# Kernel optimization log

Measured on AMD Instinct MI355X. Metric: run time of the kernel, lower is better.

Reference implementation:

```python
import jax, jax.numpy as jnp
import numpy as np

NUM_CLASSES = 24


def setup_inputs() -> dict:
    key = jax.random.key(0)
    k1, k2 = jax.random.split(key)
    data = jax.random.normal(k1, (8, 128, 128, 128), dtype=jnp.float32)
    label = jax.random.randint(k2, (8, 512, 512), 0, NUM_CLASSES, dtype=jnp.int64)
    return {"data": data, "label": label}


def reference(data, label):
    B, C, h, w = data.shape
    _, H, W = label.shape
    # nearest-neighbor interpolate to (H, W): torch 'nearest' uses floor(dst * src/dst)
    ri = (jnp.arange(H) * h) // H
    ci = (jnp.arange(W) * w) // W
    data_up = data[:, :, ri[:, None], ci[None, :]]  # [B, C, H, W]
    valid = label != -1                              # ignore mask
    lab = jnp.where(valid, label, 0)
    # scatter-add instead of one-hot + einsum (same math)
    seg = (lab + jnp.arange(B, dtype=lab.dtype)[:, None, None] * NUM_CLASSES).reshape(-1)
    x = (data_up * valid[:, None, :, :].astype(data.dtype))  # zero out ignored pixels
    x = x.transpose(0, 2, 3, 1).reshape(B * H * W, C)        # [B*H*W, C]
    sums = jax.ops.segment_sum(x, seg, num_segments=B * NUM_CLASSES)
    sums = sums.reshape(B, NUM_CLASSES, C)                   # [B, N, C]
    counts = jax.ops.segment_sum(valid.reshape(-1).astype(jnp.float32), seg,
                                 num_segments=B * NUM_CLASSES)
    counts = counts.reshape(B, NUM_CLASSES)                  # [B, N]
    feature = (sums / (counts[:, :, None] + 1e-8)).transpose(0, 2, 1)  # [B, C, N]
    mask = (counts > 0).astype(jnp.float32)                  # [B, N]
    return feature, mask
```

## Files before the change

### kernel.cpp

```cpp
#include <hip/hip_runtime.h>

#define NCLS 24
#define NB 8
#define NCH 128
#define WLO 128
#define WHI 512
#define CELLS (128*128)
#define SUBS 2
#define BPB 128
#define NBLK (NB * BPB)
#define KCH (NCLS * NCH)
#define NF (NB * KCH)

typedef _Float16 f16x4 __attribute__((ext_vector_type(4)));
typedef _Float16 f16x8 __attribute__((ext_vector_type(8)));
typedef float    f32x4 __attribute__((ext_vector_type(4)));

#define HSWZ(c_, e_) ((e_) ^ (((c_) & 7) << 3))

__global__ __launch_bounds__(256, 4)
void fm_main(const float* __restrict__ data, const int* __restrict__ label,
             _Float16* __restrict__ part, float* __restrict__ cpart)
{
    __shared__ float    histf[32 * 64];
    __shared__ _Float16 tile[NCH * 64];

    const int bid  = blockIdx.x;
    const int b    = bid >> 7;
    const int grp  = bid & 127;
    const int tid  = threadIdx.x;

    const int q    = tid & 15;
    const int chb  = tid >> 4;
    const int r    = tid >> 6;
    const int cl   = tid & 63;
    const int w    = tid >> 6;
    const int lane = tid & 63;

    const float* dbase = data  + (size_t)b * NCH * CELLS;
    const int*   lbase = label + (size_t)b * (WHI * WHI) + (size_t)(4 * grp + r) * WHI;

    float4 v[8];
    int4 lv;
    {
        const int cb = grp * WLO;
#pragma unroll
        for (int k = 0; k < 8; ++k)
            v[k] = *reinterpret_cast<const float4*>(dbase + (size_t)(chb + k * 16) * CELLS + cb + q * 4);
        lv = *reinterpret_cast<const int4*>(lbase + cl * 4);
    }

    f32x4 acc[2][2];
#pragma unroll
    for (int mt = 0; mt < 2; ++mt)
#pragma unroll
        for (int nt = 0; nt < 2; ++nt) acc[mt][nt] = (f32x4){0.f, 0.f, 0.f, 0.f};
    float cs0 = 0.f, cs1 = 0.f;

#pragma unroll
    for (int s = 0; s < SUBS; ++s) {
#pragma unroll
        for (int k = 0; k < 8; ++k) histf[tid + k * 256] = 0.f;
        __syncthreads();

        if ((unsigned)lv.x < 24u) atomicAdd(&histf[lv.x * 64 + HSWZ(lv.x, cl)], 1.f);
        if ((unsigned)lv.y < 24u) atomicAdd(&histf[lv.y * 64 + HSWZ(lv.y, cl)], 1.f);
        if ((unsigned)lv.z < 24u) atomicAdd(&histf[lv.z * 64 + HSWZ(lv.z, cl)], 1.f);
        if ((unsigned)lv.w < 24u) atomicAdd(&histf[lv.w * 64 + HSWZ(lv.w, cl)], 1.f);

#pragma unroll
        for (int k = 0; k < 8; ++k) {
            const int ch = chb + k * 16;
            f16x4 hv;
            hv[0] = (_Float16)v[k].x; hv[1] = (_Float16)v[k].y;
            hv[2] = (_Float16)v[k].z; hv[3] = (_Float16)v[k].w;
            const int idx = ch * 64 + ((((q >> 1) ^ (ch & 7)) << 3) | ((q & 1) << 2));
            *reinterpret_cast<f16x4*>(&tile[idx]) = hv;
        }

        if (s + 1 < SUBS) {
            const int cb = grp * WLO + 64;
#pragma unroll
            for (int k = 0; k < 8; ++k)
                v[k] = *reinterpret_cast<const float4*>(dbase + (size_t)(chb + k * 16) * CELLS + cb + q * 4);
            lv = *reinterpret_cast<const int4*>(lbase + 256 + cl * 4);
        }
        __syncthreads();

        f16x8 af[2][2];
#pragma unroll
        for (int mt = 0; mt < 2; ++mt)
#pragma unroll
            for (int kt = 0; kt < 2; ++kt) {
                const int cls = mt * 16 + (lane & 15);
                const int e0  = kt * 32 + (lane >> 4) * 8;
                const float* hp = &histf[cls * 64 + HSWZ(cls, e0)];
                const f32x4 h0 = *reinterpret_cast<const f32x4*>(hp);
                const f32x4 h1 = *reinterpret_cast<const f32x4*>(hp + 4);
                f16x8 a;
                a[0] = (_Float16)h0.x; a[1] = (_Float16)h0.y; a[2] = (_Float16)h0.z; a[3] = (_Float16)h0.w;
                a[4] = (_Float16)h1.x; a[5] = (_Float16)h1.y; a[6] = (_Float16)h1.z; a[7] = (_Float16)h1.w;
                af[mt][kt] = a;
                const float p = (h0.x + h0.y) + (h0.z + h0.w) + (h1.x + h1.y) + (h1.z + h1.w);
                if (mt == 0) cs0 += p; else cs1 += p;
            }

        f16x8 bf[2][2];
#pragma unroll
        for (int nt = 0; nt < 2; ++nt)
#pragma unroll
            for (int kt = 0; kt < 2; ++kt) {
                const int row = w * 32 + nt * 16 + (lane & 15);
                const int g   = kt * 4 + (lane >> 4);
                bf[nt][kt] = *reinterpret_cast<const f16x8*>(&tile[row * 64 + ((g ^ (row & 7)) << 3)]);
            }

#pragma unroll
        for (int mt = 0; mt < 2; ++mt)
#pragma unroll
            for (int nt = 0; nt < 2; ++nt)
#pragma unroll
                for (int kt = 0; kt < 2; ++kt)
                    acc[mt][nt] = __builtin_amdgcn_mfma_f32_16x16x32_f16(
                        af[mt][kt], bf[nt][kt], acc[mt][nt], 0, 0, 0);

        if (s + 1 < SUBS) __syncthreads();
    }

    cs0 += __shfl_xor(cs0, 16, 64); cs0 += __shfl_xor(cs0, 32, 64);
    cs1 += __shfl_xor(cs1, 16, 64); cs1 += __shfl_xor(cs1, 32, 64);
    if (w == 0 && lane < 16) {
        cpart[(size_t)bid * NCLS + lane] = cs0;
        if (lane < 8) cpart[(size_t)bid * NCLS + 16 + lane] = cs1;
    }

    _Float16* pblk = part + (size_t)bid * KCH;
#pragma unroll
    for (int mt = 0; mt < 2; ++mt)
#pragma unroll
        for (int nt = 0; nt < 2; ++nt)
#pragma unroll
            for (int rg = 0; rg < 4; ++rg) {
                const int cls = mt * 16 + (lane >> 4) * 4 + rg;
                const int ch  = w * 32 + nt * 16 + (lane & 15);
                if (cls < NCLS) pblk[cls * NCH + ch] = (_Float16)acc[mt][nt][rg];
            }
}

__global__ __launch_bounds__(256)
void fm_final(const _Float16* __restrict__ part, const float* __restrict__ cpart,
              float* __restrict__ out)
{
    __shared__ float red[256];
    __shared__ float credv[128];
    const int bid  = blockIdx.x;
    const int b    = bid / (NCLS * 2);
    const int rem  = bid % (NCLS * 2);
    const int cls  = rem >> 1;
    const int half = rem & 1;
    const int t    = threadIdx.x;
    const int c    = t & 63;
    const int gq   = t >> 6;

    if (t < 128) credv[t] = cpart[(size_t)(b * BPB + t) * NCLS + cls];

    const _Float16* pb = part + (size_t)(b * BPB + gq * 32) * KCH + cls * NCH + half * 64 + c;
    float s = 0.f;
#pragma unroll 8
    for (int g = 0; g < 32; ++g) s += (float)pb[(size_t)g * KCH];
    red[t] = s;
    __syncthreads();

    if (t < 64) {
        float cnt = credv[t] + credv[t + 64];
#pragma unroll
        for (int o = 32; o >= 1; o >>= 1) cnt += __shfl_xor(cnt, o, 64);
        const float sf = red[t] + red[t + 64] + red[t + 128] + red[t + 192];
        out[(size_t)b * KCH + (half * 64 + t) * NCLS + cls] = sf / (cnt + 1e-8f);
        if (t == 0 && half == 0) out[NF + b * NCLS + cls] = (cnt > 0.f) ? 1.f : 0.f;
    }
}

extern "C" void kernel_launch(void* const* d_in, const int* in_sizes, int n_in,
                              void* d_out, int out_size, void* d_ws, size_t ws_size,
                              hipStream_t stream) {
    const float* data  = (const float*)d_in[0];
    const int*   label = (const int*)d_in[1];
    float*     out   = (float*)d_out;
    _Float16*  part  = (_Float16*)d_ws;
    float*     cpart = (float*)(part + (size_t)NBLK * KCH);

    fm_main<<<dim3(NBLK), dim3(256), 0, stream>>>(data, label, part, cpart);
    fm_final<<<dim3(NB * NCLS * 2), dim3(256), 0, stream>>>(part, cpart, out);
}
```

Before: 27.37 us.

## Split label histogram into separate kernel and stream weights through global memory

```diff
diff --git a/kernel.cpp b/kernel.cpp
--- a/kernel.cpp
+++ b/kernel.cpp
@@ -3,148 +3,147 @@
 #define NCLS 24
 #define NB 8
 #define NCH 128
-#define WLO 128
 #define WHI 512
 #define CELLS (128*128)
-#define SUBS 2
-#define BPB 128
-#define NBLK (NB * BPB)
-#define KCH (NCLS * NCH)
+#define CPB 256
+#define KBLK 64
+#define NBLK (NB * KBLK)
+#define MROW 32
+#define KCH (NCH * NCLS)
 #define NF (NB * KCH)
+#define RP 129
+#define WSTR ((size_t)MROW * CELLS)
 
-typedef _Float16 f16x4 __attribute__((ext_vector_type(4)));
 typedef _Float16 f16x8 __attribute__((ext_vector_type(8)));
 typedef float    f32x4 __attribute__((ext_vector_type(4)));
 
-#define HSWZ(c_, e_) ((e_) ^ (((c_) & 7) << 3))
+__global__ __launch_bounds__(256)
+void fm_wcount(const int* __restrict__ label, _Float16* __restrict__ W,
+               float* __restrict__ cpart)
+{
+    __shared__ float h[NCLS * 257];
+    __shared__ float ps[NCLS * 8];
+    const int bid = blockIdx.x, b = bid >> 6, cblk = bid & 63;
+    const int t = threadIdx.x;
+    const int cell = cblk * 256 + t;
+    const int y = cell >> 7, x = cell & 127;
 
-__global__ __launch_bounds__(256, 4)
-void fm_main(const float* __restrict__ data, const int* __restrict__ label,
-             _Float16* __restrict__ part, float* __restrict__ cpart)
+#pragma unroll
+    for (int k = 0; k < 25; ++k) {
+        const int idx = t + k * 256;
+        if (idx < NCLS * 257) h[idx] = 0.f;
+    }
+    __syncthreads();
+
+    const int* lp = label + (size_t)b * (WHI * WHI) + (size_t)(4 * y) * WHI + 4 * x;
+    const int4 L0 = *(const int4*)lp;
+    const int4 L1 = *(const int4*)(lp + WHI);
+    const int4 L2 = *(const int4*)(lp + 2 * WHI);
+    const int4 L3 = *(const int4*)(lp + 3 * WHI);
+#define AH(v) if ((unsigned)(v) < 24u) atomicAdd(&h[(v) * 257 + t], 1.f)
+    AH(L0.x); AH(L0.y); AH(L0.z); AH(L0.w);
+    AH(L1.x); AH(L1.y); AH(L1.z); AH(L1.w);
+    AH(L2.x); AH(L2.y); AH(L2.z); AH(L2.w);
+    AH(L3.x); AH(L3.y); AH(L3.z); AH(L3.w);
+#undef AH
+
+#pragma unroll
+    for (int cls = 0; cls < NCLS; ++cls)
+        W[(size_t)b * WSTR + (size_t)cls * CELLS + cell] = (_Float16)h[cls * 257 + t];
+
+    __syncthreads();
+    if (t < 192) {
+        const int cls = t >> 3, seg = t & 7;
+        float s = 0.f;
+#pragma unroll
+        for (int m = 0; m < 32; ++m) s += h[cls * 257 + seg + 8 * m];
+        ps[cls * 8 + seg] = s;
+    }
+    __syncthreads();
+    if (t < NCLS) {
+        float s = 0.f;
+#pragma unroll
+        for (int g = 0; g < 8; ++g) s += ps[t * 8 + g];
+        cpart[bid * NCLS + t] = s;
+    }
+}
+
+__global__ __launch_bounds__(256, 2)
+void fm_gemm(const float* __restrict__ data, const _Float16* __restrict__ W,
+             _Float16* __restrict__ part)
 {
-    __shared__ float    histf[32 * 64];
-    __shared__ _Float16 tile[NCH * 64];
+    __shared__ float red[4 * MROW * RP];
+    const int bid = blockIdx.x, b = bid >> 6, kblk = bid & 63;
+    const int tid = threadIdx.x, w = tid >> 6, l = tid & 63;
+    const int l15 = l & 15, lg = l >> 4;
+    const int c0 = kblk * CPB + w * 64;
 
-    const int bid  = blockIdx.x;
-    const int b    = bid >> 7;
-    const int grp  = bid & 127;
-    const int tid  = threadIdx.x;
-
-    const int q    = tid & 15;
-    const int chb  = tid >> 4;
-    const int r    = tid >> 6;
-    const int cl   = tid & 63;
-    const int w    = tid >> 6;
-    const int lane = tid & 63;
-
-    const float* dbase = data  + (size_t)b * NCH * CELLS;
-    const int*   lbase = label + (size_t)b * (WHI * WHI) + (size_t)(4 * grp + r) * WHI;
-
-    float4 v[8];
-    int4 lv;
-    {
-        const int cb = grp * WLO;
-#pragma unroll
-        for (int k = 0; k < 8; ++k)
-            v[k] = *reinterpret_cast<const float4*>(dbase + (size_t)(chb + k * 16) * CELLS + cb + q * 4);
-        lv = *reinterpret_cast<const int4*>(lbase + cl * 4);
-    }
-
-    f32x4 acc[2][2];
+    f16x8 af[2][2];
 #pragma unroll
     for (int mt = 0; mt < 2; ++mt)
 #pragma unroll
-        for (int nt = 0; nt < 2; ++nt) acc[mt][nt] = (f32x4){0.f, 0.f, 0.f, 0.f};
-    float cs0 = 0.f, cs1 = 0.f;
+        for (int kt = 0; kt < 2; ++kt)
+            af[mt][kt] = *(const f16x8*)(W + (size_t)b * WSTR
+                                           + (size_t)(mt * 16 + l15) * CELLS
+                                           + c0 + kt * 32 + lg * 8);
 
+    f32x4 bs[2][8][2];
 #pragma unroll
-    for (int s = 0; s < SUBS; ++s) {
+    for (int kt = 0; kt < 2; ++kt)
 #pragma unroll
-        for (int k = 0; k < 8; ++k) histf[tid + k * 256] = 0.f;
-        __syncthreads();
+        for (int n = 0; n < 8; ++n)
+#pragma unroll
+            for (int p = 0; p < 2; ++p)
+                bs[kt][n][p] = *(const f32x4*)(data + (size_t)(b * NCH + n * 16 + l15) * CELLS
+                                                 + c0 + kt * 32 + lg * 8 + p * 4);
+    __builtin_amdgcn_sched_barrier(0);
 
-        if ((unsigned)lv.x < 24u) atomicAdd(&histf[lv.x * 64 + HSWZ(lv.x, cl)], 1.f);
-        if ((unsigned)lv.y < 24u) atomicAdd(&histf[lv.y * 64 + HSWZ(lv.y, cl)], 1.f);
-        if ((unsigned)lv.z < 24u) atomicAdd(&histf[lv.z * 64 + HSWZ(lv.z, cl)], 1.f);
-        if ((unsigned)lv.w < 24u) atomicAdd(&histf[lv.w * 64 + HSWZ(lv.w, cl)], 1.f);
-
-#pragma unroll
-        for (int k = 0; k < 8; ++k) {
-            const int ch = chb + k * 16;
-            f16x4 hv;
-            hv[0] = (_Float16)v[k].x; hv[1] = (_Float16)v[k].y;
-            hv[2] = (_Float16)v[k].z; hv[3] = (_Float16)v[k].w;
-            const int idx = ch * 64 + ((((q >> 1) ^ (ch & 7)) << 3) | ((q & 1) << 2));
-            *reinterpret_cast<f16x4*>(&tile[idx]) = hv;
-        }
-
-        if (s + 1 < SUBS) {
-            const int cb = grp * WLO + 64;
-#pragma unroll
-            for (int k = 0; k < 8; ++k)
-                v[k] = *reinterpret_cast<const float4*>(dbase + (size_t)(chb + k * 16) * CELLS + cb + q * 4);
-            lv = *reinterpret_cast<const int4*>(lbase + 256 + cl * 4);
-        }
-        __syncthreads();
-
-        f16x8 af[2][2];
-#pragma unroll
-        for (int mt = 0; mt < 2; ++mt)
-#pragma unroll
-            for (int kt = 0; kt < 2; ++kt) {
-                const int cls = mt * 16 + (lane & 15);
-                const int e0  = kt * 32 + (lane >> 4) * 8;
-                const float* hp = &histf[cls * 64 + HSWZ(cls, e0)];
-                const f32x4 h0 = *reinterpret_cast<const f32x4*>(hp);
-                const f32x4 h1 = *reinterpret_cast<const f32x4*>(hp + 4);
-                f16x8 a;
-                a[0] = (_Float16)h0.x; a[1] = (_Float16)h0.y; a[2] = (_Float16)h0.z; a[3] = (_Float16)h0.w;
-                a[4] = (_Float16)h1.x; a[5] = (_Float16)h1.y; a[6] = (_Float16)h1.z; a[7] = (_Float16)h1.w;
-                af[mt][kt] = a;
-                const float p = (h0.x + h0.y) + (h0.z + h0.w) + (h1.x + h1.y) + (h1.z + h1.w);
-                if (mt == 0) cs0 += p; else cs1 += p;
-            }
-
-        f16x8 bf[2][2];
-#pragma unroll
-        for (int nt = 0; nt < 2; ++nt)
-#pragma unroll
-            for (int kt = 0; kt < 2; ++kt) {
-                const int row = w * 32 + nt * 16 + (lane & 15);
-                const int g   = kt * 4 + (lane >> 4);
-                bf[nt][kt] = *reinterpret_cast<const f16x8*>(&tile[row * 64 + ((g ^ (row & 7)) << 3)]);
-            }
-
-#pragma unroll
-        for (int mt = 0; mt < 2; ++mt)
-#pragma unroll
-            for (int nt = 0; nt < 2; ++nt)
-#pragma unroll
-                for (int kt = 0; kt < 2; ++kt)
-                    acc[mt][nt] = __builtin_amdgcn_mfma_f32_16x16x32_f16(
-                        af[mt][kt], bf[nt][kt], acc[mt][nt], 0, 0, 0);
-
-        if (s + 1 < SUBS) __syncthreads();
-    }
-
-    cs0 += __shfl_xor(cs0, 16, 64); cs0 += __shfl_xor(cs0, 32, 64);
-    cs1 += __shfl_xor(cs1, 16, 64); cs1 += __shfl_xor(cs1, 32, 64);
-    if (w == 0 && lane < 16) {
-        cpart[(size_t)bid * NCLS + lane] = cs0;
-        if (lane < 8) cpart[(size_t)bid * NCLS + 16 + lane] = cs1;
-    }
-
-    _Float16* pblk = part + (size_t)bid * KCH;
+    f32x4 acc[2][8];
 #pragma unroll
     for (int mt = 0; mt < 2; ++mt)
 #pragma unroll
-        for (int nt = 0; nt < 2; ++nt)
+        for (int n = 0; n < 8; ++n) acc[mt][n] = (f32x4){0.f, 0.f, 0.f, 0.f};
+
 #pragma unroll
-            for (int rg = 0; rg < 4; ++rg) {
-                const int cls = mt * 16 + (lane >> 4) * 4 + rg;
-                const int ch  = w * 32 + nt * 16 + (lane & 15);
-                if (cls < NCLS) pblk[cls * NCH + ch] = (_Float16)acc[mt][nt][rg];
+    for (int kt = 0; kt < 2; ++kt)
+#pragma unroll
+        for (int n = 0; n < 8; ++n) {
+            f16x8 bf;
+            bf[0] = (_Float16)bs[kt][n][0].x; bf[1] = (_Float16)bs[kt][n][0].y;
+            bf[2] = (_Float16)bs[kt][n][0].z; bf[3] = (_Float16)bs[kt][n][0].w;
+            bf[4] = (_Float16)bs[kt][n][1].x; bf[5] = (_Float16)bs[kt][n][1].y;
+            bf[6] = (_Float16)bs[kt][n][1].z; bf[7] = (_Float16)bs[kt][n][1].w;
+            acc[0][n] = __builtin_amdgcn_mfma_f32_16x16x32_f16(af[0][kt], bf, acc[0][n], 0, 0, 0);
+            acc[1][n] = __builtin_amdgcn_mfma_f32_16x16x32_f16(af[1][kt], bf, acc[1][n], 0, 0, 0);
+        }
+
+    float* rw = &red[w * MROW * RP];
+#pragma unroll
+    for (int mt = 0; mt < 2; ++mt)
+#pragma unroll
+        for (int n = 0; n < 8; ++n)
+#pragma unroll
+            for (int rg = 0; rg < 4; ++rg)
+                rw[(mt * 16 + lg * 4 + rg) * RP + n * 16 + l15] = acc[mt][n][rg];
+    __syncthreads();
+
+    const int p = tid & 63, clsg = tid >> 6;
+#pragma unroll
+    for (int i = 0; i < 8; ++i) {
+        const int cls = clsg * 8 + i;
+        if (cls < NCLS) {
+            float s0 = 0.f, s1 = 0.f;
+#pragma unroll
+            for (int wv = 0; wv < 4; ++wv) {
+                s0 += red[wv * MROW * RP + cls * RP + 2 * p];
+                s1 += red[wv * MROW * RP + cls * RP + 2 * p + 1];
             }
+            const _Float16 h0 = (_Float16)s0, h1 = (_Float16)s1;
+            unsigned u = (unsigned)*(const unsigned short*)&h0
+                       | ((unsigned)*(const unsigned short*)&h1 << 16);
+            *(unsigned*)(part + (size_t)bid * 4096 + cls * 128 + 2 * p) = u;
+        }
+    }
 }
 
 __global__ __launch_bounds__(256)
@@ -152,27 +151,23 @@
               float* __restrict__ out)
 {
     __shared__ float red[256];
-    __shared__ float credv[128];
-    const int bid  = blockIdx.x;
-    const int b    = bid / (NCLS * 2);
-    const int rem  = bid % (NCLS * 2);
-    const int cls  = rem >> 1;
-    const int half = rem & 1;
-    const int t    = threadIdx.x;
-    const int c    = t & 63;
-    const int gq   = t >> 6;
+    __shared__ float credv[64];
+    const int bid = blockIdx.x;
+    const int b = bid / (NCLS * 2), rem = bid % (NCLS * 2);
+    const int cls = rem >> 1, half = rem & 1;
+    const int t = threadIdx.x, c = t & 63, gq = t >> 6;
 
-    if (t < 128) credv[t] = cpart[(size_t)(b * BPB + t) * NCLS + cls];
+    if (t < 64) credv[t] = cpart[(b * 64 + t) * NCLS + cls];
 
-    const _Float16* pb = part + (size_t)(b * BPB + gq * 32) * KCH + cls * NCH + half * 64 + c;
+    const _Float16* pb = part + (size_t)(b * 64 + gq * 16) * 4096 + cls * 128 + half * 64 + c;
     float s = 0.f;
-#pragma unroll 8
-    for (int g = 0; g < 32; ++g) s += (float)pb[(size_t)g * KCH];
+#pragma unroll
+    for (int m = 0; m < 16; ++m) s += (float)pb[(size_t)m * 4096];
     red[t] = s;
     __syncthreads();
 
     if (t < 64) {
-        float cnt = credv[t] + credv[t + 64];
+        float cnt = credv[t];
 #pragma unroll
         for (int o = 32; o >= 1; o >>= 1) cnt += __shfl_xor(cnt, o, 64);
         const float sf = red[t] + red[t + 64] + red[t + 128] + red[t + 192];
@@ -186,10 +181,13 @@
                               hipStream_t stream) {
     const float* data  = (const float*)d_in[0];
     const int*   label = (const int*)d_in[1];
-    float*     out   = (float*)d_out;
-    _Float16*  part  = (_Float16*)d_ws;
-    float*     cpart = (float*)(part + (size_t)NBLK * KCH);
+    float* out = (float*)d_out;
 
-    fm_main<<<dim3(NBLK), dim3(256), 0, stream>>>(data, label, part, cpart);
-    fm_final<<<dim3(NB * NCLS * 2), dim3(256), 0, stream>>>(part, cpart, out);
+    _Float16* W     = (_Float16*)d_ws;
+    _Float16* part  = W + (size_t)NB * WSTR;
+    float*    cpart = (float*)(part + (size_t)NBLK * 4096);
+
+    fm_wcount<<<dim3(NBLK), dim3(256), 0, stream>>>(label, W, cpart);
+    fm_gemm  <<<dim3(NBLK), dim3(256), 0, stream>>>(data, W, part);
+    fm_final <<<dim3(NB * NCLS * 2), dim3(256), 0, stream>>>(part, cpart, out);
 }
```

Result: slower. 36.36 us (+32.9%).
